# Kernel tuning notes

Measured on AMD Instinct MI355X. Metric: run time of the kernel, lower is better.

## Reference

```python
import jax, jax.numpy as jnp
import numpy as np

B, T, C, H = 4, 2048, 1024, 16
D = C // H  # head dim = 64


def setup_inputs() -> dict:
    key = jax.random.key(0)
    ks = jax.random.split(key, 9)
    s = 1.0 / np.sqrt(C)
    return {
        "x": jax.random.normal(ks[0], (B, T, C), dtype=jnp.float32),
        "Wq": jax.random.normal(ks[1], (C, C), dtype=jnp.float32) * s,
        "bq": jnp.zeros((C,), dtype=jnp.float32),
        "Wk": jax.random.normal(ks[2], (C, C), dtype=jnp.float32) * s,
        "bk": jnp.zeros((C,), dtype=jnp.float32),
        "Wv": jax.random.normal(ks[3], (C, C), dtype=jnp.float32) * s,
        "bv": jnp.zeros((C,), dtype=jnp.float32),
        "Wp": jax.random.normal(ks[4], (C, C), dtype=jnp.float32) * s,
        "bp": jnp.zeros((C,), dtype=jnp.float32),
    }


def reference(x, Wq, bq, Wk, bk, Wv, bv, Wp, bp):
    b, t, c = x.shape
    # qkv projections (torch Linear: x @ W.T + b), reshape to [B, H, T, D]
    q = (x @ Wq.T + bq).reshape(b, t, H, D).transpose(0, 2, 1, 3)
    k = (x @ Wk.T + bk).reshape(b, t, H, D).transpose(0, 2, 1, 3)
    v = (x @ Wv.T + bv).reshape(b, t, H, D).transpose(0, 2, 1, 3)
    # scaled dot-product attention with causal mask (materialized TxT, per original)
    att = jnp.einsum("bhqd,bhkd->bhqk", q, k) * (1.0 / np.sqrt(D))
    causal = jnp.tril(jnp.ones((t, t), dtype=bool))
    att = jnp.where(causal[None, None], att, jnp.float32(-jnp.inf))
    att = jax.nn.softmax(att, axis=-1)
    y = jnp.einsum("bhqk,bhkd->bhqd", att, v)
    y = y.transpose(0, 2, 1, 3).reshape(b, t, c)
    return y @ Wp.T + bp
```

## Files before the change

kernel.cpp:

```cpp
#include <hip/hip_runtime.h>
#include <stdint.h>
#include <math.h>

typedef unsigned short u16;
typedef unsigned int   u32;
typedef __attribute__((ext_vector_type(8))) short short8;
typedef __attribute__((ext_vector_type(4))) float f32x4;

#define TT 2048
#define CC 1024

__device__ __forceinline__ u16 f2bf(float f) {
  u32 u = __float_as_uint(f);
  u += 0x7fff + ((u >> 16) & 1);
  return (u16)(u >> 16);
}

__device__ __forceinline__ void gload_lds16(const void* g, void* l) {
  __builtin_amdgcn_global_load_lds((const __attribute__((address_space(1))) void*)g,
                                   (__attribute__((address_space(3))) void*)l, 16, 0, 0);
}

__device__ __forceinline__ u32 cvt_pk_bf16(float lo, float hi) {
  u32 r;
  asm("v_cvt_pk_bf16_f32 %0, %1, %2" : "=v"(r) : "v"(lo), "v"(hi));
  return r;
}

__global__ __launch_bounds__(256) void cvtk(const float* __restrict__ in,
                                            u16* __restrict__ out, int n4) {
  int i = blockIdx.x * 256 + threadIdx.x;
  if (i >= n4) return;
  float4 v = ((const float4*)in)[i];
  uint2 o;
  o.x = (u32)f2bf(v.x) | ((u32)f2bf(v.y) << 16);
  o.y = (u32)f2bf(v.z) | ((u32)f2bf(v.w) << 16);
  ((uint2*)out)[i] = o;
}

__global__ __launch_bounds__(256) void cvtW(const float* __restrict__ w0,
                                            const float* __restrict__ w1,
                                            const float* __restrict__ w2,
                                            const float* __restrict__ w3,
                                            u16* __restrict__ out) {
  int g = blockIdx.x >> 10;
  int i = (blockIdx.x & 1023) * 256 + threadIdx.x;
  const float* src = (g == 0) ? w0 : (g == 1) ? w1 : (g == 2) ? w2 : w3;
  float4 v = ((const float4*)src)[i];
  uint2 o;
  o.x = (u32)f2bf(v.x) | ((u32)f2bf(v.y) << 16);
  o.y = (u32)f2bf(v.z) | ((u32)f2bf(v.w) << 16);
  ((uint2*)(out + (size_t)g * 1048576))[i] = o;
}

__global__ __launch_bounds__(512, 2) void qk256(const u16* __restrict__ A,
                                                const u16* __restrict__ Bm,
                                                const float* __restrict__ bq,
                                                const float* __restrict__ bk,
                                                u16* __restrict__ Qo,
                                                u16* __restrict__ Ko,
                                                float qscale) {
  constexpr int NBJ = 8;
  __shared__ __align__(16) u16 lds[4][2][8192];
  const int tid = threadIdx.x;
  const int w = tid >> 6, l = tid & 63, lr = l & 15, lg = l >> 4;
  const int wm = w >> 2, wn = w & 3;
  const int nwg = gridDim.x;
  const int bid = (blockIdx.x & 7) * (nwg >> 3) + (blockIdx.x >> 3);
  const int i0 = (bid / NBJ) << 8, j0 = (bid % NBJ) << 8;

  const u16 *as0, *as1, *bs0, *bs1;
  int cd0, cd1;
  {
    int c0 = tid, c1 = tid + 512;
    int r0 = c0 >> 2, s0 = (c0 & 3) ^ ((r0 >> 1) & 3);
    int r1 = c1 >> 2, s1 = (c1 & 3) ^ ((r1 >> 1) & 3);
    as0 = A + (size_t)(i0 + r0) * 1024 + s0 * 8;
    as1 = A + (size_t)(i0 + r1) * 1024 + s1 * 8;
    bs0 = Bm + (size_t)(j0 + r0) * 1024 + s0 * 8;
    bs1 = Bm + (size_t)(j0 + r1) * 1024 + s1 * 8;
    cd0 = c0 * 8; cd1 = c1 * 8;
  }
  auto issue = [&](int t) {
    const int ko = t * 32;
    u16* la = &lds[t & 3][0][0];
    u16* lb = &lds[t & 3][1][0];
    gload_lds16(as0 + ko, la + cd0);
    gload_lds16(as1 + ko, la + cd1);
    gload_lds16(bs0 + ko, lb + cd0);
    gload_lds16(bs1 + ko, lb + cd1);
  };

  const int slot = lg ^ ((lr >> 1) & 3);
  const int sa = (((wm * 128 + lr) * 64 + slot * 16) >> 1);
  const int sb = (((wn * 64 + lr) * 64 + slot * 16) >> 1);

  f32x4 acc[8][4];
#pragma unroll
  for (int a = 0; a < 8; a++)
#pragma unroll
    for (int b = 0; b < 4; b++) acc[a][b] = f32x4{0.f, 0.f, 0.f, 0.f};

  issue(0); issue(1); issue(2);

  for (int t = 0; t < 32; ++t) {
    if (t + 3 < 32) issue(t + 3);
    if (t < 29)       asm volatile("s_waitcnt vmcnt(12)" ::: "memory");
    else if (t == 29) asm volatile("s_waitcnt vmcnt(8)" ::: "memory");
    else if (t == 30) asm volatile("s_waitcnt vmcnt(4)" ::: "memory");
    else              asm volatile("s_waitcnt vmcnt(0)" ::: "memory");
    __builtin_amdgcn_s_barrier();
    __builtin_amdgcn_sched_barrier(0);
    const u16* la = &lds[t & 3][0][0];
    const u16* lb = &lds[t & 3][1][0];
    short8 bfr[4], af[8];
#pragma unroll
    for (int ff = 0; ff < 4; ++ff) bfr[ff] = *(const short8*)&lb[sb + ff * 512];
#pragma unroll
    for (int f = 0; f < 8; ++f) af[f] = *(const short8*)&la[sa + f * 512];
    asm volatile("s_waitcnt lgkmcnt(0)" ::: "memory");
    __builtin_amdgcn_s_barrier();
    __builtin_amdgcn_sched_barrier(0);
#pragma unroll
    for (int f = 0; f < 8; ++f)
#pragma unroll
      for (int ff = 0; ff < 4; ++ff)
        acc[f][ff] = __builtin_amdgcn_mfma_f32_16x16x32_bf16(af[f], bfr[ff], acc[f][ff], 0, 0, 0);
  }

  const int mat = j0 >> 10;
  const float* bias = mat ? bk : bq;
  u16* outp = mat ? Ko : Qo;
  const float sc = mat ? 1.0f : qscale;
  const int jjb = j0 & 1023;
#pragma unroll
  for (int f = 0; f < 8; ++f)
#pragma unroll
    for (int ff = 0; ff < 4; ++ff) {
      int jq = jjb + wn * 64 + ff * 16 + lr;
      float bv = bias[jq];
      int h = jq >> 6, d = jq & 63;
#pragma unroll
      for (int j2 = 0; j2 < 4; ++j2) {
        int i = i0 + wm * 128 + f * 16 + lg * 4 + j2;
        float v = (acc[f][ff][j2] + bv) * sc;
        outp[(size_t)((i >> 11) * 16 + h) * 131072 + (i & 2047) * 64 + d] = f2bf(v);
      }
    }
}

template <int MODE>
__global__ __launch_bounds__(256) void gemm_bt(const u16* __restrict__ A,
                                               const u16* __restrict__ Bm,
                                               const float* __restrict__ bias,
                                               void* __restrict__ outp,
                                               int M, int N, float scale) {
  constexpr int K = 1024;
  __shared__ __align__(16) u16 ldsA[2][128 * 32];
  __shared__ __align__(16) u16 ldsB[2][128 * 32];
  const int tid = threadIdx.x;
  const int w = tid >> 6, l = tid & 63;
  const int lr = l & 15, lg = l >> 4;
  const int nbj = N >> 7;
  const int nwg = gridDim.x;
  const int bid = (blockIdx.x & 7) * (nwg >> 3) + (blockIdx.x >> 3);
  const int i0 = (bid / nbj) << 7;
  const int j0 = (bid % nbj) << 7;
  const int wr = w >> 1, wc = w & 1;

  f32x4 acc[4][4];
#pragma unroll
  for (int a = 0; a < 4; a++)
#pragma unroll
    for (int b = 0; b < 4; b++) acc[a][b] = f32x4{0.f, 0.f, 0.f, 0.f};

  auto stage = [&](int buf, int kt) {
    const u16* sA = A + (size_t)i0 * K + kt * 32;
    const u16* sB = Bm + (size_t)j0 * K + kt * 32;
#pragma unroll
    for (int i = 0; i < 2; ++i) {
      int chunk = w * 128 + i * 64 + l;
      int r = chunk >> 2;
      int co = (chunk & 3) * 8;
      gload_lds16(sA + (size_t)r * K + co, &ldsA[buf][chunk * 8]);
      gload_lds16(sB + (size_t)r * K + co, &ldsB[buf][chunk * 8]);
    }
  };

  stage(0, 0);
  __syncthreads();
  int cur = 0;
  for (int kt = 0; kt < 32; ++kt) {
    if (kt + 1 < 32) stage(cur ^ 1, kt + 1);
    short8 af[4], bfr[4];
#pragma unroll
    for (int f = 0; f < 4; ++f) {
      af[f]  = *(const short8*)&ldsA[cur][(wr * 64 + f * 16 + lr) * 32 + lg * 8];
      bfr[f] = *(const short8*)&ldsB[cur][(wc * 64 + f * 16 + lr) * 32 + lg * 8];
    }
#pragma unroll
    for (int fi = 0; fi < 4; ++fi)
#pragma unroll
      for (int fj = 0; fj < 4; ++fj)
        acc[fi][fj] = __builtin_amdgcn_mfma_f32_16x16x32_bf16(af[fi], bfr[fj], acc[fi][fj], 0, 0, 0);
    __syncthreads();
    cur ^= 1;
  }

#pragma unroll
  for (int fi = 0; fi < 4; ++fi) {
#pragma unroll
    for (int fj = 0; fj < 4; ++fj) {
#pragma unroll
      for (int j2 = 0; j2 < 4; ++j2) {
        int i = i0 + wr * 64 + fi * 16 + lg * 4 + j2;
        int j = j0 + wc * 64 + fj * 16 + lr;
        float v = (acc[fi][fj][j2] + (MODE == 1 ? bias[i] : bias[j])) * scale;
        if constexpr (MODE == 1) {
          ((u16*)outp)[(size_t)i * 8192 + j] = f2bf(v);
        } else {
          ((float*)outp)[(size_t)i * 1024 + j] = v;
        }
      }
    }
  }
}

__global__ __launch_bounds__(256, 4) void attn_fwd(const u16* __restrict__ Q,
                                                   const u16* __restrict__ Kt,
                                                   const u16* __restrict__ VT,
                                                   u16* __restrict__ Y) {
  const int bid = blockIdx.x;
  const int bh = bid & 63;
  const int p  = bid >> 6;
  const int b = bh >> 4, h = bh & 15;
  const int w = threadIdx.x >> 6, l = threadIdx.x & 63;
  const int lr = l & 15, lg = l >> 4;

  const u16* Qh = Q + (size_t)bh * (TT * 64);
  const u16* Kh = Kt + (size_t)bh * (TT * 64);
  const u16* Vh = VT + (size_t)(h * 64) * (4 * TT) + (size_t)b * TT;

  __shared__ __align__(16) u16 ldsK[2][32 * 128];
  __shared__ __align__(16) u16 ldsV[2][32 * 128];
  __shared__ __align__(16) u16 plds[4][16 * 64];
  u16* pw = &plds[w][0];

  const int nA = p + 1;
  const int tileB = 31 - p;

  const u16 *ks0, *ks1, *vs0, *vs1;
  int cd0, cd1;
  {
    int c0 = threadIdx.x, c1 = threadIdx.x + 256;
    int r0 = c0 >> 4, sw0 = (c0 & 15) ^ (r0 & 15);
    int r1 = c1 >> 4, sw1 = (c1 & 15) ^ (r1 & 15);
    int kl0 = 2 * r0 + (sw0 >> 3), co0 = (sw0 & 7) * 8;
    int kl1 = 2 * r1 + (sw1 >> 3), co1 = (sw1 & 7) * 8;
    ks0 = Kh + (size_t)kl0 * 64 + co0;
    ks1 = Kh + (size_t)kl1 * 64 + co1;
    vs0 = Vh + (size_t)kl0 * (4 * TT) + co0;
    vs1 = Vh + (size_t)kl1 * (4 * TT) + co1;
    cd0 = c0 * 8; cd1 = c1 * 8;
  }
  auto stageKV = [&](int buf, int kc0) {
    gload_lds16(ks0 + (size_t)kc0 * 64, &ldsK[buf][cd0]);
    gload_lds16(ks1 + (size_t)kc0 * 64, &ldsK[buf][cd1]);
    gload_lds16(vs0 + kc0, &ldsV[buf][cd0]);
    gload_lds16(vs1 + kc0, &ldsV[buf][cd1]);
  };

  int kof[4][2], vof[4][2];
#pragma unroll
  for (int fk = 0; fk < 4; ++fk)
#pragma unroll
    for (int fd = 0; fd < 2; ++fd) {
      int kl = fk * 16 + lr;
      int r2 = kl >> 1;
      int b2 = (((kl & 1) << 7) | (fd * 64 + lg * 16)) ^ ((r2 & 15) << 4);
      kof[fk][fd] = r2 * 128 + (b2 >> 1);
    }
#pragma unroll
  for (int fd = 0; fd < 4; ++fd)
#pragma unroll
    for (int ks = 0; ks < 2; ++ks) {
      int dl = fd * 16 + lr;
      int r2 = dl >> 1;
      int b2 = (((dl & 1) << 7) | (ks * 64 + lg * 16)) ^ ((r2 & 15) << 4);
      vof[fd][ks] = r2 * 128 + (b2 >> 1);
    }
  int pwo[4], pro[2];
#pragma unroll
  for (int fk = 0; fk < 4; ++fk)
    pwo[fk] = lr * 64 + ((fk * 16 + lg * 4) ^ ((lr & 7) << 3));
#pragma unroll
  for (int ks = 0; ks < 2; ++ks)
    pro[ks] = lr * 64 + ((ks * 32 + lg * 8) ^ ((lr & 7) << 3));

  short8 qf[2];
  f32x4 ot[4];
  float lsum;
  int q0;
  auto loadQ = [&](int tile) {
    q0 = tile * 64 + w * 16;
#pragma unroll
    for (int fd = 0; fd < 2; ++fd)
      qf[fd] = *(const short8*)&Qh[(size_t)(q0 + lr) * 64 + fd * 32 + lg * 8];
#pragma unroll
    for (int fd = 0; fd < 4; ++fd) ot[fd] = f32x4{0.f, 0.f, 0.f, 0.f};
    lsum = 0.f;
  };
  auto epilogue = [&]() {
    float ls = lsum;
    ls += __shfl_xor(ls, 16);
    ls += __shfl_xor(ls, 32);
    float inv = 1.0f / ls;
    const int q = q0 + lr;
#pragma unroll
    for (int fd = 0; fd < 4; ++fd) {
      uint2 o;
      o.x = cvt_pk_bf16(ot[fd][0] * inv, ot[fd][1] * inv);
      o.y = cvt_pk_bf16(ot[fd][2] * inv, ot[fd][3] * inv);
      *(uint2*)&Y[(size_t)(b * TT + q) * CC + h * 64 + fd * 16 + lg * 4] = o;
    }
  };

  loadQ(p);
  stageKV(0, 0);
  __syncthreads();
  int cur = 0;
  for (int u = 0; u < 33; ++u) {
    const bool inA = u < nA;
    const int kt = inA ? u : u - nA;
    const int kc0 = kt << 6;
    if (u + 1 < 33) {
      int kt2 = (u + 1 < nA) ? u + 1 : u + 1 - nA;
      stageKV(cur ^ 1, kt2 << 6);
    }
    const u16* lk = &ldsK[cur][0];
    const u16* lv = &ldsV[cur][0];
    f32x4 st[4];
#pragma unroll
    for (int a = 0; a < 4; a++) st[a] = f32x4{0.f, 0.f, 0.f, 0.f};
#pragma unroll
    for (int fd = 0; fd < 2; ++fd)
#pragma unroll
      for (int fk = 0; fk < 4; ++fk)
        st[fk] = __builtin_amdgcn_mfma_f32_16x16x32_bf16(*(const short8*)&lk[kof[fk][fd]],
                                                         qf[fd], st[fk], 0, 0, 0);
    if ((u == nA - 1) || (u == 32)) {
      const int q = q0 + lr;
#pragma unroll
      for (int fk = 0; fk < 4; ++fk)
#pragma unroll
        for (int j = 0; j < 4; ++j) {
          int k = kc0 + fk * 16 + lg * 4 + j;
          if (k > q) st[fk][j] = -1e30f;
        }
    }
    float ls = 0.f;
#pragma unroll
    for (int fk = 0; fk < 4; ++fk) {
      float p0 = exp2f(st[fk][0]);
      float p1 = exp2f(st[fk][1]);
      float p2 = exp2f(st[fk][2]);
      float p3 = exp2f(st[fk][3]);
      ls += (p0 + p1) + (p2 + p3);
      uint2 pk2;
      pk2.x = cvt_pk_bf16(p0, p1);
      pk2.y = cvt_pk_bf16(p2, p3);
      *(uint2*)&pw[pwo[fk]] = pk2;
    }
    lsum += ls;
    asm volatile("s_waitcnt lgkmcnt(0)" ::: "memory");
    __builtin_amdgcn_sched_barrier(0);
#pragma unroll
    for (int ks = 0; ks < 2; ++ks) {
      short8 pf = *(const short8*)&pw[pro[ks]];
#pragma unroll
      for (int fd = 0; fd < 4; ++fd)
        ot[fd] = __builtin_amdgcn_mfma_f32_16x16x32_bf16(*(const short8*)&lv[vof[fd][ks]],
                                                         pf, ot[fd], 0, 0, 0);
    }
    __syncthreads();
    cur ^= 1;
    if (u == nA - 1) {
      epilogue();
      loadQ(tileB);
    }
  }
  epilogue();
}

extern "C" void kernel_launch(void* const* d_in, const int* in_sizes, int n_in,
                              void* d_out, int out_size, void* d_ws, size_t ws_size,
                              hipStream_t stream) {
  const float* x  = (const float*)d_in[0];
  const float* Wq = (const float*)d_in[1];
  const float* bq = (const float*)d_in[2];
  const float* Wk = (const float*)d_in[3];
  const float* bk = (const float*)d_in[4];
  const float* Wv = (const float*)d_in[5];
  const float* bv = (const float*)d_in[6];
  const float* Wp = (const float*)d_in[7];
  const float* bp = (const float*)d_in[8];
  float* out = (float*)d_out;

  u16* ws  = (u16*)d_ws;
  u16* xb  = ws;
  u16* wqb = xb + 8388608;
  u16* wkb = wqb + 1048576;
  u16* wvb = wkb + 1048576;
  u16* wpb = wvb + 1048576;
  u16* Qb  = wpb + 1048576;
  u16* Kb  = Qb + 8388608;
  u16* VTb = Kb + 8388608;
  u16* Yb  = xb;

  cvtk<<<8192, 256, 0, stream>>>(x, xb, 2097152);
  cvtW<<<4096, 256, 0, stream>>>(Wq, Wk, Wv, Wp, wqb);

  qk256<<<256, 512, 0, stream>>>(xb, wqb, bq, bk, Qb, Kb,
                                 0.125f * 1.44269504088896340736f);
  gemm_bt<1><<<512, 256, 0, stream>>>(wvb, xb, bv, VTb, 1024, 8192, 1.0f);

  attn_fwd<<<1024, 256, 0, stream>>>(Qb, Kb, VTb, Yb);

  gemm_bt<2><<<512, 256, 0, stream>>>(Yb, wpb, bp, out, 8192, 1024, 1.0f);
}
```

Before: 270.0 us.

## Compute softmax row sums via MFMA with ones, raw v_exp, and setprio around MFMAs

Replaces the scalar per-lane accumulation of softmax denominators and the cross-lane shuffle reduction with an extra MFMA that multiplies the bf16 probability tile by a ones vector, so the sum lands already reduced in the accumulator. exp2f is swapped for the raw v_exp_f32 instruction to avoid library range handling. s_setprio raises wave priority around the MFMA blocks in both the projection GEMM and attention loops so matrix work from different waves interleaves better. Row sums now come from bf16-rounded probabilities, which changes numerics slightly but keeps the normalization consistent with what is multiplied by V.

```diff
diff --git a/kernel.cpp b/kernel.cpp
--- a/kernel.cpp
+++ b/kernel.cpp
@@ -24,6 +24,12 @@
 __device__ __forceinline__ u32 cvt_pk_bf16(float lo, float hi) {
   u32 r;
   asm("v_cvt_pk_bf16_f32 %0, %1, %2" : "=v"(r) : "v"(lo), "v"(hi));
+  return r;
+}
+
+__device__ __forceinline__ float expv(float x) {
+  float r;
+  asm("v_exp_f32 %0, %1" : "=v"(r) : "v"(x));
   return r;
 }
 
@@ -121,11 +127,13 @@
     asm volatile("s_waitcnt lgkmcnt(0)" ::: "memory");
     __builtin_amdgcn_s_barrier();
     __builtin_amdgcn_sched_barrier(0);
+    __builtin_amdgcn_s_setprio(1);
 #pragma unroll
     for (int f = 0; f < 8; ++f)
 #pragma unroll
       for (int ff = 0; ff < 4; ++ff)
         acc[f][ff] = __builtin_amdgcn_mfma_f32_16x16x32_bf16(af[f], bfr[ff], acc[f][ff], 0, 0, 0);
+    __builtin_amdgcn_s_setprio(0);
   }
 
   const int mat = j0 >> 10;
@@ -297,9 +305,13 @@
   for (int ks = 0; ks < 2; ++ks)
     pro[ks] = lr * 64 + ((ks * 32 + lg * 8) ^ ((lr & 7) << 3));
 
+  short8 onesf;
+#pragma unroll
+  for (int i = 0; i < 8; ++i) onesf[i] = (short)0x3F80;
+
   short8 qf[2];
   f32x4 ot[4];
-  float lsum;
+  f32x4 lsacc;
   int q0;
   auto loadQ = [&](int tile) {
     q0 = tile * 64 + w * 16;
@@ -308,13 +320,10 @@
       qf[fd] = *(const short8*)&Qh[(size_t)(q0 + lr) * 64 + fd * 32 + lg * 8];
 #pragma unroll
     for (int fd = 0; fd < 4; ++fd) ot[fd] = f32x4{0.f, 0.f, 0.f, 0.f};
-    lsum = 0.f;
+    lsacc = f32x4{0.f, 0.f, 0.f, 0.f};
   };
   auto epilogue = [&]() {
-    float ls = lsum;
-    ls += __shfl_xor(ls, 16);
-    ls += __shfl_xor(ls, 32);
-    float inv = 1.0f / ls;
+    float inv = 1.0f / lsacc[0];
     const int q = q0 + lr;
 #pragma unroll
     for (int fd = 0; fd < 4; ++fd) {
@@ -342,12 +351,14 @@
     f32x4 st[4];
 #pragma unroll
     for (int a = 0; a < 4; a++) st[a] = f32x4{0.f, 0.f, 0.f, 0.f};
+    __builtin_amdgcn_s_setprio(1);
 #pragma unroll
     for (int fd = 0; fd < 2; ++fd)
 #pragma unroll
       for (int fk = 0; fk < 4; ++fk)
         st[fk] = __builtin_amdgcn_mfma_f32_16x16x32_bf16(*(const short8*)&lk[kof[fk][fd]],
                                                          qf[fd], st[fk], 0, 0, 0);
+    __builtin_amdgcn_s_setprio(0);
     if ((u == nA - 1) || (u == 32)) {
       const int q = q0 + lr;
 #pragma unroll
@@ -358,30 +369,26 @@
           if (k > q) st[fk][j] = -1e30f;
         }
     }
-    float ls = 0.f;
 #pragma unroll
     for (int fk = 0; fk < 4; ++fk) {
-      float p0 = exp2f(st[fk][0]);
-      float p1 = exp2f(st[fk][1]);
-      float p2 = exp2f(st[fk][2]);
-      float p3 = exp2f(st[fk][3]);
-      ls += (p0 + p1) + (p2 + p3);
       uint2 pk2;
-      pk2.x = cvt_pk_bf16(p0, p1);
-      pk2.y = cvt_pk_bf16(p2, p3);
+      pk2.x = cvt_pk_bf16(expv(st[fk][0]), expv(st[fk][1]));
+      pk2.y = cvt_pk_bf16(expv(st[fk][2]), expv(st[fk][3]));
       *(uint2*)&pw[pwo[fk]] = pk2;
     }
-    lsum += ls;
     asm volatile("s_waitcnt lgkmcnt(0)" ::: "memory");
     __builtin_amdgcn_sched_barrier(0);
+    __builtin_amdgcn_s_setprio(1);
 #pragma unroll
     for (int ks = 0; ks < 2; ++ks) {
       short8 pf = *(const short8*)&pw[pro[ks]];
+      lsacc = __builtin_amdgcn_mfma_f32_16x16x32_bf16(onesf, pf, lsacc, 0, 0, 0);
 #pragma unroll
       for (int fd = 0; fd < 4; ++fd)
         ot[fd] = __builtin_amdgcn_mfma_f32_16x16x32_bf16(*(const short8*)&lv[vof[fd][ks]],
                                                          pf, ot[fd], 0, 0, 0);
     }
+    __builtin_amdgcn_s_setprio(0);
     __syncthreads();
     cur ^= 1;
     if (u == nA - 1) {
```

Result: faster. 256.4 us (-5.0%).
